# Kernel optimization log

Measured on AMD Instinct MI355X. Metric: run time of the kernel, lower is better.

## Reference

```python
import jax, jax.numpy as jnp
import numpy as np

K = 3      # kernel size
PAD = 1    # padding


def setup_inputs() -> dict:
    key = jax.random.key(0)
    k1, k2, k3, k4 = jax.random.split(key, 4)
    B, C, H, W, O = 8, 3, 512, 512, 16
    x = jax.random.normal(k1, (B, C, H, W), dtype=jnp.float32)
    offsets = jax.random.normal(k2, (B, 2 * K * K, H, W), dtype=jnp.float32)
    weight = jax.random.normal(k3, (O, C, K, K), dtype=jnp.float32) * 0.1
    bias = jax.random.normal(k4, (O,), dtype=jnp.float32) * 0.1
    return {"x": x, "offsets": offsets, "weight": weight, "bias": bias}


def _deform_conv2d(x, offsets, weight, bias):
    # x: [B,C,H,W]; offsets: [B,2*K*K,H,W] with (dy,dx) interleaved per tap
    B, C, H, W = x.shape
    KK = K * K
    ky = jnp.arange(KK) // K
    kx = jnp.arange(KK) % K
    # base sampling grid (stride=1, dilation=1): p = out_pos - PAD + tap
    base_y = (ky[:, None, None] - PAD + jnp.arange(H)[None, :, None]).astype(x.dtype)  # [KK,H,1]
    base_x = (kx[:, None, None] - PAD + jnp.arange(W)[None, None, :]).astype(x.dtype)  # [KK,1,W]
    py = offsets[:, 0::2] + base_y[None]  # [B,KK,H,W]
    px = offsets[:, 1::2] + base_x[None]  # [B,KK,H,W]

    def sample(img, py_b, px_b):  # img [C,H,W]; py_b,px_b [KK,H,W]
        y0 = jnp.floor(py_b)
        x0 = jnp.floor(px_b)
        wy = py_b - y0  # fractional parts
        wx = px_b - x0
        y0i = y0.astype(jnp.int32)
        x0i = x0.astype(jnp.int32)

        def gather(yi, xi):
            valid = (yi >= 0) & (yi < H) & (xi >= 0) & (xi < W)
            yc = jnp.clip(yi, 0, H - 1)
            xc = jnp.clip(xi, 0, W - 1)
            return img[:, yc, xc] * valid[None].astype(img.dtype)  # [C,KK,H,W]

        v00 = gather(y0i, x0i)
        v01 = gather(y0i, x0i + 1)
        v10 = gather(y0i + 1, x0i)
        v11 = gather(y0i + 1, x0i + 1)
        return (v00 * ((1 - wy) * (1 - wx))[None]
                + v01 * ((1 - wy) * wx)[None]
                + v10 * (wy * (1 - wx))[None]
                + v11 * (wy * wx)[None])

    sampled = jax.vmap(sample)(x, py, px)  # [B,C,KK,H,W]
    O = weight.shape[0]
    out = jnp.einsum('bckhw,ock->bohw', sampled, weight.reshape(O, C, KK))
    return out + bias[None, :, None, None]


def reference(x, offsets, weight, bias):
    return _deform_conv2d(x, offsets, weight, bias)
```

## Files before the change

### kernel.cpp

```cpp
#include <hip/hip_runtime.h>


#define Bc 8
#define Cc 3
#define Hc 512
#define Wc 512
#define Oc 16
#define HWc (512 * 512)
#define KKc 9

__global__ __launch_bounds__(256) void transpose_kernel(
    const float* __restrict__ x, float4* __restrict__ xt) {
  int pix = blockIdx.x * 256 + threadIdx.x;
  int b = pix >> 18;
  int hw = pix & (HWc - 1);
  const float* xb = x + b * (Cc * HWc) + hw;
  float4 v;
  v.x = xb[0];
  v.y = xb[HWc];
  v.z = xb[2 * HWc];
  v.w = 0.f;
  xt[pix] = v;
}

__global__ __launch_bounds__(256, 4) void dcn_main(
    const float4* __restrict__ xt,
    const float* __restrict__ offsets,
    const float* __restrict__ weight,
    const float* __restrict__ bias,
    float* __restrict__ out) {
  int pix = blockIdx.x * 256 + threadIdx.x;
  int b = pix >> 18;
  int hw = pix & (HWc - 1);
  int h = hw >> 9;
  int w = hw & 511;

  const float4* xb = xt + (b << 18);
  const float* ob = offsets + b * (2 * KKc * HWc) + hw;

  const float fh = (float)(h - 1);
  const float fw = (float)(w - 1);

  int addr[KKc][4];
  float wt[KKc][4];
#pragma unroll
  for (int kk = 0; kk < KKc; ++kk) {
    const int ky = kk / 3;
    const int kx = kk % 3;
    float oy = __builtin_nontemporal_load(&ob[(2 * kk) * HWc]);
    float ox = __builtin_nontemporal_load(&ob[(2 * kk + 1) * HWc]);
    float py = oy + fh + (float)ky;
    float px = ox + fw + (float)kx;
    float y0f = floorf(py);
    float x0f = floorf(px);
    float wy = py - y0f;
    float wx = px - x0f;
    int y0 = (int)y0f;
    int x0 = (int)x0f;
    int y1 = y0 + 1;
    int x1 = x0 + 1;

    float vy0 = ((unsigned)y0 < (unsigned)Hc) ? 1.f : 0.f;
    float vy1 = ((unsigned)y1 < (unsigned)Hc) ? 1.f : 0.f;
    float vx0 = ((unsigned)x0 < (unsigned)Wc) ? 1.f : 0.f;
    float vx1 = ((unsigned)x1 < (unsigned)Wc) ? 1.f : 0.f;
    float wy0 = 1.f - wy;
    float wx0 = 1.f - wx;
    wt[kk][0] = (wy0 * wx0) * (vy0 * vx0);
    wt[kk][1] = (wy0 * wx) * (vy0 * vx1);
    wt[kk][2] = (wy * wx0) * (vy1 * vx0);
    wt[kk][3] = (wy * wx) * (vy1 * vx1);

    int y0c = min(max(y0, 0), Hc - 1);
    int y1c = min(max(y1, 0), Hc - 1);
    int x0c = min(max(x0, 0), Wc - 1);
    int x1c = min(max(x1, 0), Wc - 1);
    addr[kk][0] = (y0c << 9) + x0c;
    addr[kk][1] = (y0c << 9) + x1c;
    addr[kk][2] = (y1c << 9) + x0c;
    addr[kk][3] = (y1c << 9) + x1c;
  }

  float acc[Oc];
#pragma unroll
  for (int o = 0; o < Oc; ++o) acc[o] = bias[o];

#pragma unroll
  for (int kk = 0; kk < KKc; ++kk) {
    float4 v00 = xb[addr[kk][0]];
    float4 v01 = xb[addr[kk][1]];
    float4 v10 = xb[addr[kk][2]];
    float4 v11 = xb[addr[kk][3]];
    float w00 = wt[kk][0], w01 = wt[kk][1], w10 = wt[kk][2], w11 = wt[kk][3];

    float val0 = v00.x * w00 + v01.x * w01 + v10.x * w10 + v11.x * w11;
    float val1 = v00.y * w00 + v01.y * w01 + v10.y * w10 + v11.y * w11;
    float val2 = v00.z * w00 + v01.z * w01 + v10.z * w10 + v11.z * w11;

    const float* wk = weight + kk;
#pragma unroll
    for (int o = 0; o < Oc; ++o) {
      acc[o] = fmaf(wk[o * 27 + 0], val0,
               fmaf(wk[o * 27 + 9], val1,
               fmaf(wk[o * 27 + 18], val2, acc[o])));
    }
  }

  float* op = out + b * (Oc * HWc) + hw;
#pragma unroll
  for (int o = 0; o < Oc; ++o)
    __builtin_nontemporal_store(acc[o], &op[o * HWc]);
}

__global__ __launch_bounds__(256) void dcn_fallback(
    const float* __restrict__ x,
    const float* __restrict__ offsets,
    const float* __restrict__ weight,
    const float* __restrict__ bias,
    float* __restrict__ out) {
  int pix = blockIdx.x * 256 + threadIdx.x;
  int b = pix >> 18;
  int hw = pix & (HWc - 1);
  int h = hw >> 9;
  int w = hw & 511;
  const float* xb = x + b * (Cc * HWc);
  const float* ob = offsets + b * (2 * KKc * HWc) + hw;
  float acc[Oc];
#pragma unroll
  for (int o = 0; o < Oc; ++o) acc[o] = bias[o];
  const float fh = (float)(h - 1);
  const float fw = (float)(w - 1);
#pragma unroll
  for (int kk = 0; kk < KKc; ++kk) {
    const int ky = kk / 3;
    const int kx = kk % 3;
    float oy = ob[(2 * kk) * HWc];
    float ox = ob[(2 * kk + 1) * HWc];
    float py = oy + fh + (float)ky;
    float px = ox + fw + (float)kx;
    float y0f = floorf(py), x0f = floorf(px);
    float wy = py - y0f, wx = px - x0f;
    int y0 = (int)y0f, x0 = (int)x0f, y1 = y0 + 1, x1 = x0 + 1;
    float vy0 = ((unsigned)y0 < (unsigned)Hc) ? 1.f : 0.f;
    float vy1 = ((unsigned)y1 < (unsigned)Hc) ? 1.f : 0.f;
    float vx0 = ((unsigned)x0 < (unsigned)Wc) ? 1.f : 0.f;
    float vx1 = ((unsigned)x1 < (unsigned)Wc) ? 1.f : 0.f;
    float wy0 = 1.f - wy, wx0 = 1.f - wx;
    float w00 = (wy0 * wx0) * (vy0 * vx0);
    float w01 = (wy0 * wx) * (vy0 * vx1);
    float w10 = (wy * wx0) * (vy1 * vx0);
    float w11 = (wy * wx) * (vy1 * vx1);
    int y0c = min(max(y0, 0), Hc - 1);
    int y1c = min(max(y1, 0), Hc - 1);
    int x0c = min(max(x0, 0), Wc - 1);
    int x1c = min(max(x1, 0), Wc - 1);
    int a00 = (y0c << 9) + x0c, a01 = (y0c << 9) + x1c;
    int a10 = (y1c << 9) + x0c, a11 = (y1c << 9) + x1c;
    float val[Cc];
#pragma unroll
    for (int c = 0; c < Cc; ++c) {
      const float* xc = xb + c * HWc;
      val[c] = xc[a00] * w00 + xc[a01] * w01 + xc[a10] * w10 + xc[a11] * w11;
    }
    const float* wk = weight + kk;
#pragma unroll
    for (int o = 0; o < Oc; ++o)
#pragma unroll
      for (int c = 0; c < Cc; ++c)
        acc[o] = fmaf(wk[o * 27 + c * 9], val[c], acc[o]);
  }
  float* op = out + b * (Oc * HWc) + hw;
#pragma unroll
  for (int o = 0; o < Oc; ++o) op[o * HWc] = acc[o];
}

extern "C" void kernel_launch(void* const* d_in, const int* in_sizes, int n_in,
                              void* d_out, int out_size, void* d_ws, size_t ws_size,
                              hipStream_t stream) {
  const float* x = (const float*)d_in[0];
  const float* offsets = (const float*)d_in[1];
  const float* weight = (const float*)d_in[2];
  const float* bias = (const float*)d_in[3];
  float* out = (float*)d_out;

  const int total = Bc * HWc;
  const size_t xt_bytes = (size_t)total * 16;
  dim3 grid(total / 256), block(256);

  if (ws_size >= xt_bytes) {
    float4* xt = (float4*)d_ws;
    hipLaunchKernelGGL(transpose_kernel, grid, block, 0, stream, x, xt);
    hipLaunchKernelGGL(dcn_main, grid, block, 0, stream,
                       (const float4*)xt, offsets, weight, bias, out);
  } else {
    hipLaunchKernelGGL(dcn_fallback, grid, block, 0, stream,
                       x, offsets, weight, bias, out);
  }
}
```

Measured before the change: 369.2 us.

## Process four pixels per thread with prefetched offsets and batched gathers

The main deformable-conv kernel now assigns one image row per 128-thread block, and each thread handles four pixels strided by 128. Offsets for the next tap are prefetched while the current tap runs, and all 16 gathers for a tap are issued before the math, with a sched_barrier to keep that order. The goal is more memory-level parallelism and amortised weight loads per FMA. The cost is much higher register pressure, since 64 accumulators plus 16 float4 values are live, which may lower occupancy.

```diff
diff --git a/kernel.cpp b/kernel.cpp
--- a/kernel.cpp
+++ b/kernel.cpp
@@ -23,93 +23,121 @@
   xt[pix] = v;
 }
 
-__global__ __launch_bounds__(256, 4) void dcn_main(
+__global__ __launch_bounds__(128, 2) void dcn_main4(
     const float4* __restrict__ xt,
     const float* __restrict__ offsets,
     const float* __restrict__ weight,
     const float* __restrict__ bias,
     float* __restrict__ out) {
-  int pix = blockIdx.x * 256 + threadIdx.x;
-  int b = pix >> 18;
-  int hw = pix & (HWc - 1);
-  int h = hw >> 9;
-  int w = hw & 511;
-
-  const float4* xb = xt + (b << 18);
-  const float* ob = offsets + b * (2 * KKc * HWc) + hw;
-
+  const int row = blockIdx.x;
+  const int b = row >> 9;
+  const int h = row & 511;
+  const int l = threadIdx.x;
+
+  const float4* __restrict__ xtb = xt + ((size_t)b << 18);
+  const float* __restrict__ ob =
+      offsets + (size_t)b * (2 * KKc * HWc) + (h << 9) + l;
   const float fh = (float)(h - 1);
-  const float fw = (float)(w - 1);
-
-  int addr[KKc][4];
-  float wt[KKc][4];
+
+  float acc[Oc][4];
+#pragma unroll
+  for (int o = 0; o < Oc; ++o) {
+    float bo = bias[o];
+#pragma unroll
+    for (int p = 0; p < 4; ++p) acc[o][p] = bo;
+  }
+
+  float oy[4], ox[4], oyN[4], oxN[4];
+#pragma unroll
+  for (int p = 0; p < 4; ++p) {
+    oy[p] = __builtin_nontemporal_load(ob + 0 * HWc + (p << 7));
+    ox[p] = __builtin_nontemporal_load(ob + 1 * HWc + (p << 7));
+  }
+
 #pragma unroll
   for (int kk = 0; kk < KKc; ++kk) {
     const int ky = kk / 3;
     const int kx = kk % 3;
-    float oy = __builtin_nontemporal_load(&ob[(2 * kk) * HWc]);
-    float ox = __builtin_nontemporal_load(&ob[(2 * kk + 1) * HWc]);
-    float py = oy + fh + (float)ky;
-    float px = ox + fw + (float)kx;
-    float y0f = floorf(py);
-    float x0f = floorf(px);
-    float wy = py - y0f;
-    float wx = px - x0f;
-    int y0 = (int)y0f;
-    int x0 = (int)x0f;
-    int y1 = y0 + 1;
-    int x1 = x0 + 1;
-
-    float vy0 = ((unsigned)y0 < (unsigned)Hc) ? 1.f : 0.f;
-    float vy1 = ((unsigned)y1 < (unsigned)Hc) ? 1.f : 0.f;
-    float vx0 = ((unsigned)x0 < (unsigned)Wc) ? 1.f : 0.f;
-    float vx1 = ((unsigned)x1 < (unsigned)Wc) ? 1.f : 0.f;
-    float wy0 = 1.f - wy;
-    float wx0 = 1.f - wx;
-    wt[kk][0] = (wy0 * wx0) * (vy0 * vx0);
-    wt[kk][1] = (wy0 * wx) * (vy0 * vx1);
-    wt[kk][2] = (wy * wx0) * (vy1 * vx0);
-    wt[kk][3] = (wy * wx) * (vy1 * vx1);
-
-    int y0c = min(max(y0, 0), Hc - 1);
-    int y1c = min(max(y1, 0), Hc - 1);
-    int x0c = min(max(x0, 0), Wc - 1);
-    int x1c = min(max(x1, 0), Wc - 1);
-    addr[kk][0] = (y0c << 9) + x0c;
-    addr[kk][1] = (y0c << 9) + x1c;
-    addr[kk][2] = (y1c << 9) + x0c;
-    addr[kk][3] = (y1c << 9) + x1c;
-  }
-
-  float acc[Oc];
-#pragma unroll
-  for (int o = 0; o < Oc; ++o) acc[o] = bias[o];
-
-#pragma unroll
-  for (int kk = 0; kk < KKc; ++kk) {
-    float4 v00 = xb[addr[kk][0]];
-    float4 v01 = xb[addr[kk][1]];
-    float4 v10 = xb[addr[kk][2]];
-    float4 v11 = xb[addr[kk][3]];
-    float w00 = wt[kk][0], w01 = wt[kk][1], w10 = wt[kk][2], w11 = wt[kk][3];
-
-    float val0 = v00.x * w00 + v01.x * w01 + v10.x * w10 + v11.x * w11;
-    float val1 = v00.y * w00 + v01.y * w01 + v10.y * w10 + v11.y * w11;
-    float val2 = v00.z * w00 + v01.z * w01 + v10.z * w10 + v11.z * w11;
-
-    const float* wk = weight + kk;
-#pragma unroll
-    for (int o = 0; o < Oc; ++o) {
-      acc[o] = fmaf(wk[o * 27 + 0], val0,
-               fmaf(wk[o * 27 + 9], val1,
-               fmaf(wk[o * 27 + 18], val2, acc[o])));
-    }
-  }
-
-  float* op = out + b * (Oc * HWc) + hw;
+
+    if (kk < KKc - 1) {
+#pragma unroll
+      for (int p = 0; p < 4; ++p) {
+        oyN[p] = __builtin_nontemporal_load(ob + (2 * kk + 2) * HWc + (p << 7));
+        oxN[p] = __builtin_nontemporal_load(ob + (2 * kk + 3) * HWc + (p << 7));
+      }
+    }
+
+    float wt[4][4];
+    int ad[4][4];
+#pragma unroll
+    for (int p = 0; p < 4; ++p) {
+      float py = oy[p] + fh + (float)ky;
+      float px = ox[p] + (float)(l + (p << 7) - 1 + kx);
+      float y0f = floorf(py);
+      float x0f = floorf(px);
+      float wy = py - y0f;
+      float wx = px - x0f;
+      int y0 = (int)y0f;
+      int x0 = (int)x0f;
+      int y1 = y0 + 1;
+      int x1 = x0 + 1;
+      float vy0 = ((unsigned)y0 < (unsigned)Hc) ? 1.f : 0.f;
+      float vy1 = ((unsigned)y1 < (unsigned)Hc) ? 1.f : 0.f;
+      float vx0 = ((unsigned)x0 < (unsigned)Wc) ? 1.f : 0.f;
+      float vx1 = ((unsigned)x1 < (unsigned)Wc) ? 1.f : 0.f;
+      float wy0 = 1.f - wy;
+      float wx0 = 1.f - wx;
+      wt[p][0] = (wy0 * wx0) * (vy0 * vx0);
+      wt[p][1] = (wy0 * wx) * (vy0 * vx1);
+      wt[p][2] = (wy * wx0) * (vy1 * vx0);
+      wt[p][3] = (wy * wx) * (vy1 * vx1);
+      int y0c = min(max(y0, 0), Hc - 1);
+      int y1c = min(max(y1, 0), Hc - 1);
+      int x0c = min(max(x0, 0), Wc - 1);
+      int x1c = min(max(x1, 0), Wc - 1);
+      ad[p][0] = (y0c << 9) + x0c;
+      ad[p][1] = (y0c << 9) + x1c;
+      ad[p][2] = (y1c << 9) + x0c;
+      ad[p][3] = (y1c << 9) + x1c;
+    }
+
+    float4 v[4][4];
+#pragma unroll
+    for (int p = 0; p < 4; ++p) {
+      v[p][0] = xtb[ad[p][0]];
+      v[p][1] = xtb[ad[p][1]];
+      v[p][2] = xtb[ad[p][2]];
+      v[p][3] = xtb[ad[p][3]];
+    }
+    __builtin_amdgcn_sched_barrier(0);
+
+#pragma unroll
+    for (int p = 0; p < 4; ++p) {
+      float w00 = wt[p][0], w01 = wt[p][1], w10 = wt[p][2], w11 = wt[p][3];
+      float val0 = v[p][0].x * w00 + v[p][1].x * w01 + v[p][2].x * w10 + v[p][3].x * w11;
+      float val1 = v[p][0].y * w00 + v[p][1].y * w01 + v[p][2].y * w10 + v[p][3].y * w11;
+      float val2 = v[p][0].z * w00 + v[p][1].z * w01 + v[p][2].z * w10 + v[p][3].z * w11;
+      const float* wk = weight + kk;
+#pragma unroll
+      for (int o = 0; o < Oc; ++o) {
+        acc[o][p] = fmaf(wk[o * 27 + 0], val0,
+                    fmaf(wk[o * 27 + 9], val1,
+                    fmaf(wk[o * 27 + 18], val2, acc[o][p])));
+      }
+    }
+
+    if (kk < KKc - 1) {
+#pragma unroll
+      for (int p = 0; p < 4; ++p) { oy[p] = oyN[p]; ox[p] = oxN[p]; }
+    }
+  }
+
+  float* op = out + (size_t)b * (Oc * HWc) + (h << 9) + l;
 #pragma unroll
   for (int o = 0; o < Oc; ++o)
-    __builtin_nontemporal_store(acc[o], &op[o * HWc]);
+#pragma unroll
+    for (int p = 0; p < 4; ++p)
+      __builtin_nontemporal_store(acc[o][p], &op[o * HWc + (p << 7)]);
 }
 
 __global__ __launch_bounds__(256) void dcn_fallback(
@@ -132,12 +160,9 @@
   const float fw = (float)(w - 1);
 #pragma unroll
   for (int kk = 0; kk < KKc; ++kk) {
-    const int ky = kk / 3;
-    const int kx = kk % 3;
-    float oy = ob[(2 * kk) * HWc];
-    float ox = ob[(2 * kk + 1) * HWc];
-    float py = oy + fh + (float)ky;
-    float px = ox + fw + (float)kx;
+    const int ky = kk / 3, kx = kk % 3;
+    float py = ob[(2 * kk) * HWc] + fh + (float)ky;
+    float px = ob[(2 * kk + 1) * HWc] + fw + (float)kx;
     float y0f = floorf(py), x0f = floorf(px);
     float wy = py - y0f, wx = px - x0f;
     int y0 = (int)y0f, x0 = (int)x0f, y1 = y0 + 1, x1 = x0 + 1;
@@ -185,15 +210,14 @@
 
   const int total = Bc * HWc;
   const size_t xt_bytes = (size_t)total * 16;
-  dim3 grid(total / 256), block(256);
 
   if (ws_size >= xt_bytes) {
     float4* xt = (float4*)d_ws;
-    hipLaunchKernelGGL(transpose_kernel, grid, block, 0, stream, x, xt);
-    hipLaunchKernelGGL(dcn_main, grid, block, 0, stream,
+    hipLaunchKernelGGL(transpose_kernel, dim3(total / 256), dim3(256), 0, stream, x, xt);
+    hipLaunchKernelGGL(dcn_main4, dim3(Bc * Hc), dim3(128), 0, stream,
                        (const float4*)xt, offsets, weight, bias, out);
   } else {
-    hipLaunchKernelGGL(dcn_fallback, grid, block, 0, stream,
+    hipLaunchKernelGGL(dcn_fallback, dim3(total / 256), dim3(256), 0, stream,
                        x, offsets, weight, bias, out);
   }
 }
```

New measurement: 857.2 us. 132% more time.
